# Kernel tuning notes

Measured on AMD Instinct MI355X. Metric: run time of the kernel, lower is better.

Reference implementation:

```python
import jax, jax.numpy as jnp
import numpy as np

B, M, D = 32768, 4096, 128


def setup_inputs() -> dict:
    key = jax.random.key(0)
    k1, k2 = jax.random.split(key)
    local_stats = jax.random.normal(k1, (B, D), dtype=jnp.float32)
    memory = jax.random.normal(k2, (M, D), dtype=jnp.float32)
    return {"local_stats": local_stats, "memory": memory}


def reference(local_stats, memory):
    # attention logits: [B, M] = x @ memory^T (unscaled single-head attention read)
    logits = jnp.einsum("bd,md->bm", local_stats, memory)
    attn = jax.nn.softmax(logits, axis=1)          # [B, M]
    global_stats = jnp.einsum("bm,md->bd", attn, memory)  # [B, D]
    return global_stats
```

## Files before the change

### kernel.cpp

```cpp
#include <hip/hip_runtime.h>
#include <hip/hip_bf16.h>
#include <stdint.h>


typedef float    f32x16 __attribute__((ext_vector_type(16)));
typedef _Float16 f16x8  __attribute__((ext_vector_type(8)));
typedef uint32_t u32;

#define AS1 __attribute__((address_space(1)))
#define AS3 __attribute__((address_space(3)))

#define D_DIM 128
#define B_ROWS 32768
#define KTILE_HW 4096
#define HALF_TILES 64

#if __has_builtin(__builtin_amdgcn_exp2f)
#define EXP2F(x) __builtin_amdgcn_exp2f(x)
#else
#define EXP2F(x) exp2f(x)
#endif

__device__ __forceinline__ uint16_t f32_to_f16_bits(float x) {
    _Float16 h = (_Float16)x;
    uint16_t r; __builtin_memcpy(&r, &h, 2);
    return r;
}

__global__ void prep_frags(const float* __restrict__ mem,
                           uint16_t* __restrict__ kws,
                           uint16_t* __restrict__ vws) {
    int t = blockIdx.x * blockDim.x + threadIdx.x;
    int lane = t & 63;
    int fi = t >> 6;
    int f8 = fi & 7, mt = fi >> 3;
    size_t base = (size_t)mt * KTILE_HW;
    {
        int m  = mt * 32 + (lane & 31);
        int d0 = f8 * 16 + (lane >> 5) * 8;
        const float* src = mem + (size_t)m * D_DIM + d0;
        #pragma unroll
        for (int e = 0; e < 8; ++e)
            kws[base + f8 * 512 + lane * 8 + e] = f32_to_f16_bits(src[e]);
    }
    {
        int dt = fi & 3, ks = (fi >> 2) & 1;
        int d  = dt * 32 + (lane & 31);
        int m0 = mt * 32 + ks * 16 + (lane >> 5) * 8;
        #pragma unroll
        for (int e = 0; e < 8; ++e)
            vws[base + f8 * 512 + lane * 8 + e] =
                f32_to_f16_bits(mem[(size_t)(m0 + e) * D_DIM + d]);
    }
}


#define STAGE_K(t_, wb_) do {                                                 \
    const char* g_ = (const char*)(kws + (size_t)(tilebase + (t_)) * KTILE_HW);\
    char* l_ = (char*)&sbuf[wb_][0];                                          \
    _Pragma("unroll")                                                         \
    for (int j_ = 0; j_ < 2; ++j_) {                                          \
        int ch_ = wave * 2 + j_;                                              \
        __builtin_amdgcn_global_load_lds(                                     \
            (const AS1 char*)(g_ + ch_ * 1024 + lane * 16),                   \
            (AS3 char*)(l_ + ch_ * 1024), 16, 0, 0);                          \
    }                                                                         \
} while (0)

#define MFMA_F16(a_, b_, c_) __builtin_amdgcn_mfma_f32_32x32x16_f16(a_, b_, c_, 0, 0, 0)

#define VLOAD(t_, vf_) do {                                                   \
    const uint16_t* vg_ = vws + (size_t)(tilebase + (t_)) * KTILE_HW + lane * 8;\
    _Pragma("unroll")                                                         \
    for (int f_ = 0; f_ < 8; ++f_)                                            \
        vf_[f_] = *(const f16x8*)(vg_ + f_ * 512);                            \
} while (0)

#define QK(bp_, s_) do {                                                      \
    f16x8 kh_[8];                                                             \
    _Pragma("unroll")                                                         \
    for (int kk_ = 0; kk_ < 8; ++kk_)                                         \
        kh_[kk_] = *(const f16x8*)((bp_) + kk_ * 512);                        \
    f32x16 sA_, sB_;                                                          \
    _Pragma("unroll")                                                         \
    for (int i_ = 0; i_ < 16; ++i_) { sA_[i_] = 0.f; sB_[i_] = 0.f; }         \
    sA_ = MFMA_F16(kh_[0], qh[0], sA_);                                       \
    sB_ = MFMA_F16(kh_[1], qh[1], sB_);                                       \
    sA_ = MFMA_F16(kh_[2], qh[2], sA_);                                       \
    sB_ = MFMA_F16(kh_[3], qh[3], sB_);                                       \
    sA_ = MFMA_F16(kh_[4], qh[4], sA_);                                       \
    sB_ = MFMA_F16(kh_[5], qh[5], sB_);                                       \
    sA_ = MFMA_F16(kh_[6], qh[6], sA_);                                       \
    sB_ = MFMA_F16(kh_[7], qh[7], sB_);                                       \
    s_ = sA_ + sB_;                                                           \
} while (0)

#define SMX_PV(s_, vf_) do {                                                  \
    float a0=fmaxf(s_[0],s_[1]),  a1=fmaxf(s_[2],s_[3]);                      \
    float a2=fmaxf(s_[4],s_[5]),  a3=fmaxf(s_[6],s_[7]);                      \
    float a4=fmaxf(s_[8],s_[9]),  a5=fmaxf(s_[10],s_[11]);                    \
    float a6=fmaxf(s_[12],s_[13]),a7=fmaxf(s_[14],s_[15]);                    \
    float tmax = fmaxf(fmaxf(fmaxf(a0,a1),fmaxf(a2,a3)),                      \
                       fmaxf(fmaxf(a4,a5),fmaxf(a6,a7)));                     \
    tmax = fmaxf(tmax, __shfl_xor(tmax, 32));                                 \
    if (__any(tmax > m_run + 8.0f)) {                    \
        float mn = fmaxf(m_run, tmax);                                        \
        float fr = EXP2F(m_run - mn);                                         \
        m_run = mn; l_run *= fr;                                              \
        _Pragma("unroll")                                                     \
        for (int r_ = 0; r_ < 16; ++r_) {                                     \
            O0[r_] *= fr; O1[r_] *= fr; O2[r_] *= fr; O3[r_] *= fr;           \
        }                                                                     \
    }                                                                         \
    _Pragma("unroll")                                                         \
    for (int r_ = 0; r_ < 16; ++r_) s_[r_] = EXP2F(s_[r_] - m_run);           \
    { float q0s=s_[0]+s_[1],  q1s=s_[2]+s_[3],  q2s=s_[4]+s_[5],  q3s=s_[6]+s_[7];   \
      float q4s=s_[8]+s_[9],  q5s=s_[10]+s_[11],q6s=s_[12]+s_[13],q7s=s_[14]+s_[15]; \
      l_run += ((q0s+q1s)+(q2s+q3s)) + ((q4s+q5s)+(q6s+q7s)); }               \
    u32 c_[8];                                                                \
    _Pragma("unroll")                                                         \
    for (int j_ = 0; j_ < 8; ++j_)                                            \
        asm("v_cvt_pkrtz_f16_f32 %0, %1, %2"                                  \
            : "=v"(c_[j_]) : "v"(s_[2*j_]), "v"(s_[2*j_+1]));                 \
    asm("v_permlane32_swap_b32 %0, %1" : "+v"(c_[0]), "+v"(c_[2]));           \
    asm("v_permlane32_swap_b32 %0, %1" : "+v"(c_[1]), "+v"(c_[3]));           \
    asm("v_permlane32_swap_b32 %0, %1" : "+v"(c_[4]), "+v"(c_[6]));           \
    asm("v_permlane32_swap_b32 %0, %1" : "+v"(c_[5]), "+v"(c_[7]));           \
    f16x8 pf0_, pf1_;                                                         \
    { u32 w_[4] = {c_[0], c_[1], c_[2], c_[3]}; __builtin_memcpy(&pf0_, w_, 16); } \
    { u32 w_[4] = {c_[4], c_[5], c_[6], c_[7]}; __builtin_memcpy(&pf1_, w_, 16); } \
    O0 = MFMA_F16(vf_[0], pf0_, O0);                                          \
    O1 = MFMA_F16(vf_[1], pf0_, O1);                                          \
    O2 = MFMA_F16(vf_[2], pf0_, O2);                                          \
    O3 = MFMA_F16(vf_[3], pf0_, O3);                                          \
    O0 = MFMA_F16(vf_[4], pf1_, O0);                                          \
    O1 = MFMA_F16(vf_[5], pf1_, O1);                                          \
    O2 = MFMA_F16(vf_[6], pf1_, O2);                                          \
    O3 = MFMA_F16(vf_[7], pf1_, O3);                                          \
} while (0)

#define PSTORE_TILE(Ot_, t_) do {                                             \
    _Pragma("unroll")                                                         \
    for (int g_ = 0; g_ < 4; ++g_) {                                          \
        float4 v_ = { Ot_[4*g_+0], Ot_[4*g_+1], Ot_[4*g_+2], Ot_[4*g_+3] };   \
        int d_ = (t_) * 32 + 8 * g_ + 4 * hi32;                               \
        *(float4*)(prow + d_) = v_;                                           \
    }                                                                         \
} while (0)

__global__ __launch_bounds__(256, 2)
void attn_main(const float* __restrict__ qin,
               const uint16_t* __restrict__ kws,
               const uint16_t* __restrict__ vws,
               float* __restrict__ out0,
               float* __restrict__ pout1,
               float2* __restrict__ pml) {
    __shared__ uint16_t sbuf[4][KTILE_HW];

    const int lane = threadIdx.x & 63;
    const int wave = threadIdx.x >> 6;
    const int half = blockIdx.x & 1;
    const int tilebase = half * HALF_TILES;
    const int q0   = (blockIdx.x >> 1) * 128 + wave * 32;
    const int qrow = q0 + (lane & 31);
    const int hi32 = lane >> 5;

    f16x8 qh[8];
    {
        const float LOG2E = 1.44269504088896340736f;
        #pragma unroll
        for (int kk = 0; kk < 8; ++kk) {
            const float* src = qin + (size_t)qrow * D_DIM + kk * 16 + hi32 * 8;
            float4 a = *(const float4*)(src);
            float4 b = *(const float4*)(src + 4);
            float xs[8] = {a.x, a.y, a.z, a.w, b.x, b.y, b.z, b.w};
            #pragma unroll
            for (int e = 0; e < 8; ++e)
                qh[kk][e] = (_Float16)(xs[e] * LOG2E);
        }
    }

    f32x16 O0, O1, O2, O3;
    #pragma unroll
    for (int i = 0; i < 16; ++i) { O0[i]=0.f; O1[i]=0.f; O2[i]=0.f; O3[i]=0.f; }
    float m_run = -1e30f, l_run = 0.f;

    STAGE_K(0, 0);
    STAGE_K(1, 1);
    __syncthreads();

    #pragma unroll 1
    for (int t = 0; t < HALF_TILES; t += 2) {
        if (t + 2 < HALF_TILES) STAGE_K(t + 2, (t + 2) & 3);
        if (t + 3 < HALF_TILES) STAGE_K(t + 3, (t + 3) & 3);
        const uint16_t* bp0 = &sbuf[t & 3][0] + lane * 8;
        const uint16_t* bp1 = &sbuf[(t + 1) & 3][0] + lane * 8;

        f16x8 vf0[8], vf1[8];
        VLOAD(t, vf0);
        VLOAD(t + 1, vf1);

        f32x16 s0, s1;
        QK(bp0, s0);
        QK(bp1, s1);
        SMX_PV(s0, vf0);
        SMX_PV(s1, vf1);
        __syncthreads();
    }

    l_run += __shfl_xor(l_run, 32);
    float* prow = (half == 0 ? out0 : pout1) + (size_t)qrow * D_DIM;
    PSTORE_TILE(O0, 0); PSTORE_TILE(O1, 1);
    PSTORE_TILE(O2, 2); PSTORE_TILE(O3, 3);
    if (lane < 32) {
        pml[(size_t)half * B_ROWS + qrow] = make_float2(m_run, l_run);
    }
}

__global__ __launch_bounds__(256)
void merge_halves(const float* __restrict__ pout1,
                  const float2* __restrict__ pml,
                  float* __restrict__ out) {
    int idx  = blockIdx.x * 256 + threadIdx.x;
    int row  = idx >> 5;
    int c4   = idx & 31;
    float2 a = pml[row];
    float2 b = pml[B_ROWS + row];
    float mn = fmaxf(a.x, b.x);
    float wa = EXP2F(a.x - mn);
    float wb = EXP2F(b.x - mn);
    float rinv = 1.0f / (a.y * wa + b.y * wb);
    float4* O = (float4*)(out + (size_t)row * D_DIM) + c4;
    const float4* P1 = (const float4*)(pout1 + (size_t)row * D_DIM) + c4;
    float4 p0 = *O, p1 = *P1;
    float4 v;
    v.x = (p0.x * wa + p1.x * wb) * rinv;
    v.y = (p0.y * wa + p1.y * wb) * rinv;
    v.z = (p0.z * wa + p1.z * wb) * rinv;
    v.w = (p0.w * wa + p1.w * wb) * rinv;
    *O = v;
}

extern "C" void kernel_launch(void* const* d_in, const int* in_sizes, int n_in,
                              void* d_out, int out_size, void* d_ws, size_t ws_size,
                              hipStream_t stream) {
    const float* local_stats = (const float*)d_in[0];
    const float* memory      = (const float*)d_in[1];
    float* out = (float*)d_out;

    uint16_t* kws  = (uint16_t*)d_ws;
    uint16_t* vws  = kws + 128 * KTILE_HW;
    float*   pout1 = (float*)((char*)d_ws + 2 * 1024 * 1024);
    float2*  pml   = (float2*)((char*)pout1 + (size_t)B_ROWS * D_DIM * 4);

    prep_frags<<<256, 256, 0, stream>>>(memory, kws, vws);
    attn_main<<<512, 256, 0, stream>>>(local_stats, kws, vws, out, pout1, pml);
    merge_halves<<<4096, 256, 0, stream>>>(pout1, pml, out);
}
```

Before: 102.7 us.

## Load K fragments directly from global into registers, drop LDS staging

Removes the shared-memory ring buffer and the async global_load_lds staging of K tiles. K fragments are now loaded straight from global memory into registers, double-buffered one tile ahead, and the per-iteration __syncthreads is gone. MFMA sections are also wrapped in s_setprio to raise wave priority during matrix work. The trade-off is higher register pressure and no LDS sharing of K across the four waves, so global/L2 traffic per block for K goes up fourfold.

```diff
diff --git a/kernel.cpp b/kernel.cpp
--- a/kernel.cpp
+++ b/kernel.cpp
@@ -6,9 +6,6 @@
 typedef float    f32x16 __attribute__((ext_vector_type(16)));
 typedef _Float16 f16x8  __attribute__((ext_vector_type(8)));
 typedef uint32_t u32;
-
-#define AS1 __attribute__((address_space(1)))
-#define AS3 __attribute__((address_space(3)))
 
 #define D_DIM 128
 #define B_ROWS 32768
@@ -55,47 +52,38 @@
 }
 
 
-#define STAGE_K(t_, wb_) do {                                                 \
-    const char* g_ = (const char*)(kws + (size_t)(tilebase + (t_)) * KTILE_HW);\
-    char* l_ = (char*)&sbuf[wb_][0];                                          \
-    _Pragma("unroll")                                                         \
-    for (int j_ = 0; j_ < 2; ++j_) {                                          \
-        int ch_ = wave * 2 + j_;                                              \
-        __builtin_amdgcn_global_load_lds(                                     \
-            (const AS1 char*)(g_ + ch_ * 1024 + lane * 16),                   \
-            (AS3 char*)(l_ + ch_ * 1024), 16, 0, 0);                          \
-    }                                                                         \
-} while (0)
-
 #define MFMA_F16(a_, b_, c_) __builtin_amdgcn_mfma_f32_32x32x16_f16(a_, b_, c_, 0, 0, 0)
 
-#define VLOAD(t_, vf_) do {                                                   \
-    const uint16_t* vg_ = vws + (size_t)(tilebase + (t_)) * KTILE_HW + lane * 8;\
+#define KLOAD(kp_, KH) do {                                                   \
+    _Pragma("unroll")                                                         \
+    for (int kk_ = 0; kk_ < 8; ++kk_)                                         \
+        KH[kk_] = *(const f16x8*)((kp_) + kk_ * 512);                         \
+} while (0)
+
+#define VLOAD(vp_, VF) do {                                                   \
     _Pragma("unroll")                                                         \
     for (int f_ = 0; f_ < 8; ++f_)                                            \
-        vf_[f_] = *(const f16x8*)(vg_ + f_ * 512);                            \
-} while (0)
-
-#define QK(bp_, s_) do {                                                      \
-    f16x8 kh_[8];                                                             \
-    _Pragma("unroll")                                                         \
-    for (int kk_ = 0; kk_ < 8; ++kk_)                                         \
-        kh_[kk_] = *(const f16x8*)((bp_) + kk_ * 512);                        \
+        VF[f_] = *(const f16x8*)((vp_) + f_ * 512);                           \
+} while (0)
+
+#define QK(KH, s_) do {                                                       \
     f32x16 sA_, sB_;                                                          \
     _Pragma("unroll")                                                         \
     for (int i_ = 0; i_ < 16; ++i_) { sA_[i_] = 0.f; sB_[i_] = 0.f; }         \
-    sA_ = MFMA_F16(kh_[0], qh[0], sA_);                                       \
-    sB_ = MFMA_F16(kh_[1], qh[1], sB_);                                       \
-    sA_ = MFMA_F16(kh_[2], qh[2], sA_);                                       \
-    sB_ = MFMA_F16(kh_[3], qh[3], sB_);                                       \
-    sA_ = MFMA_F16(kh_[4], qh[4], sA_);                                       \
-    sB_ = MFMA_F16(kh_[5], qh[5], sB_);                                       \
-    sA_ = MFMA_F16(kh_[6], qh[6], sA_);                                       \
-    sB_ = MFMA_F16(kh_[7], qh[7], sB_);                                       \
+    __builtin_amdgcn_s_setprio(1);                                            \
+    sA_ = MFMA_F16(KH[0], qh[0], sA_);                                        \
+    sB_ = MFMA_F16(KH[1], qh[1], sB_);                                        \
+    sA_ = MFMA_F16(KH[2], qh[2], sA_);                                        \
+    sB_ = MFMA_F16(KH[3], qh[3], sB_);                                        \
+    sA_ = MFMA_F16(KH[4], qh[4], sA_);                                        \
+    sB_ = MFMA_F16(KH[5], qh[5], sB_);                                        \
+    sA_ = MFMA_F16(KH[6], qh[6], sA_);                                        \
+    sB_ = MFMA_F16(KH[7], qh[7], sB_);                                        \
+    __builtin_amdgcn_s_setprio(0);                                            \
     s_ = sA_ + sB_;                                                           \
 } while (0)
 
-#define SMX_PV(s_, vf_) do {                                                  \
+#define SMX_PV(s_, VF) do {                                                   \
     float a0=fmaxf(s_[0],s_[1]),  a1=fmaxf(s_[2],s_[3]);                      \
     float a2=fmaxf(s_[4],s_[5]),  a3=fmaxf(s_[6],s_[7]);                      \
     float a4=fmaxf(s_[8],s_[9]),  a5=fmaxf(s_[10],s_[11]);                    \
@@ -129,14 +117,16 @@
     f16x8 pf0_, pf1_;                                                         \
     { u32 w_[4] = {c_[0], c_[1], c_[2], c_[3]}; __builtin_memcpy(&pf0_, w_, 16); } \
     { u32 w_[4] = {c_[4], c_[5], c_[6], c_[7]}; __builtin_memcpy(&pf1_, w_, 16); } \
-    O0 = MFMA_F16(vf_[0], pf0_, O0);                                          \
-    O1 = MFMA_F16(vf_[1], pf0_, O1);                                          \
-    O2 = MFMA_F16(vf_[2], pf0_, O2);                                          \
-    O3 = MFMA_F16(vf_[3], pf0_, O3);                                          \
-    O0 = MFMA_F16(vf_[4], pf1_, O0);                                          \
-    O1 = MFMA_F16(vf_[5], pf1_, O1);                                          \
-    O2 = MFMA_F16(vf_[6], pf1_, O2);                                          \
-    O3 = MFMA_F16(vf_[7], pf1_, O3);                                          \
+    __builtin_amdgcn_s_setprio(1);                                            \
+    O0 = MFMA_F16(VF[0], pf0_, O0);                                           \
+    O1 = MFMA_F16(VF[1], pf0_, O1);                                           \
+    O2 = MFMA_F16(VF[2], pf0_, O2);                                           \
+    O3 = MFMA_F16(VF[3], pf0_, O3);                                           \
+    O0 = MFMA_F16(VF[4], pf1_, O0);                                           \
+    O1 = MFMA_F16(VF[5], pf1_, O1);                                           \
+    O2 = MFMA_F16(VF[6], pf1_, O2);                                           \
+    O3 = MFMA_F16(VF[7], pf1_, O3);                                           \
+    __builtin_amdgcn_s_setprio(0);                                            \
 } while (0)
 
 #define PSTORE_TILE(Ot_, t_) do {                                             \
@@ -155,8 +145,6 @@
                float* __restrict__ out0,
                float* __restrict__ pout1,
                float2* __restrict__ pml) {
-    __shared__ uint16_t sbuf[4][KTILE_HW];
-
     const int lane = threadIdx.x & 63;
     const int wave = threadIdx.x >> 6;
     const int half = blockIdx.x & 1;
@@ -185,27 +173,32 @@
     for (int i = 0; i < 16; ++i) { O0[i]=0.f; O1[i]=0.f; O2[i]=0.f; O3[i]=0.f; }
     float m_run = -1e30f, l_run = 0.f;
 
-    STAGE_K(0, 0);
-    STAGE_K(1, 1);
-    __syncthreads();
+    const uint16_t* kp = kws + (size_t)tilebase * KTILE_HW + lane * 8;
+    const uint16_t* vp = vws + (size_t)tilebase * KTILE_HW + lane * 8;
+
+    f16x8 khA[8], khB[8];
+    KLOAD(kp, khA);
 
     #pragma unroll 1
-    for (int t = 0; t < HALF_TILES; t += 2) {
-        if (t + 2 < HALF_TILES) STAGE_K(t + 2, (t + 2) & 3);
-        if (t + 3 < HALF_TILES) STAGE_K(t + 3, (t + 3) & 3);
-        const uint16_t* bp0 = &sbuf[t & 3][0] + lane * 8;
-        const uint16_t* bp1 = &sbuf[(t + 1) & 3][0] + lane * 8;
-
-        f16x8 vf0[8], vf1[8];
-        VLOAD(t, vf0);
-        VLOAD(t + 1, vf1);
-
-        f32x16 s0, s1;
-        QK(bp0, s0);
-        QK(bp1, s1);
-        SMX_PV(s0, vf0);
-        SMX_PV(s1, vf1);
-        __syncthreads();
+    for (int tp = 0; tp < HALF_TILES / 2; ++tp) {
+        const int t = 2 * tp;
+        {
+            f16x8 vf[8];
+            VLOAD(vp + (size_t)t * KTILE_HW, vf);
+            KLOAD(kp + (size_t)(t + 1) * KTILE_HW, khB);
+            f32x16 s;
+            QK(khA, s);
+            SMX_PV(s, vf);
+        }
+        {
+            f16x8 vf[8];
+            VLOAD(vp + (size_t)(t + 1) * KTILE_HW, vf);
+            if (t + 2 < HALF_TILES)
+                KLOAD(kp + (size_t)(t + 2) * KTILE_HW, khA);
+            f32x16 s;
+            QK(khB, s);
+            SMX_PV(s, vf);
+        }
     }
 
     l_run += __shfl_xor(l_run, 32);
```

New measurement: 109.3 us. 6.4% more time.
